# Optimization experiments

Hardware: AMD Instinct MI355X
Metric: run time of the kernel (lower is better)

The kernel has to match this reference:

```python
import jax, jax.numpy as jnp
import numpy as np

ALPHA = 0.15
CLIP = 5.0
EPS = 1e-6
LN_EPS = 1e-5

B, S, D, F = 4, 4096, 2048, 128


def setup_inputs() -> dict:
    key = jax.random.key(0)
    ks = jax.random.split(key, 8)
    sd = lambda fan_in: 1.0 / np.sqrt(fan_in)
    return {
        "x": jax.random.normal(ks[0], (B, S, D), dtype=jnp.float32),
        "Q_w": jax.random.normal(ks[1], (D, F), dtype=jnp.float32) * sd(D),
        "Q_b": jnp.zeros((F,), jnp.float32),
        "K_w": jax.random.normal(ks[2], (D, F), dtype=jnp.float32) * sd(D),
        "K_b": jnp.zeros((F,), jnp.float32),
        "lo_proj_w": jax.random.normal(ks[3], (D, D), dtype=jnp.float32) * sd(D),
        "lo_proj_b": jnp.zeros((D,), jnp.float32),
        "lo_p_w": jax.random.normal(ks[4], (D, F), dtype=jnp.float32) * sd(D),
        "lo_p_b": jnp.zeros((F,), jnp.float32),
        "proj_w": jax.random.normal(ks[5], (F, D), dtype=jnp.float32) * sd(F),
        "proj_b": jnp.zeros((D,), jnp.float32),
        "O_w": jax.random.normal(ks[6], (D // 2, D), dtype=jnp.float32) * sd(D // 2),
        "O_b": jnp.zeros((D,), jnp.float32),
        "ln_gamma": jnp.ones((D,), jnp.float32),
        "ln_beta": jnp.zeros((D,), jnp.float32),
    }


def _ema_over_time(score):
    # score: [B, S, F]; ema[0]=score[0]; ema[t]=a*score[t]+(1-a)*ema[t-1]
    seq = jnp.swapaxes(score, 0, 1)  # [S, B, F]

    def step(prev, x_t):
        new = ALPHA * x_t + (1.0 - ALPHA) * prev
        return new, new

    init = seq[0]
    _, rest = jax.lax.scan(step, init, seq[1:])
    ema_seq = jnp.concatenate([init[None], rest], axis=0)
    return jnp.swapaxes(ema_seq, 0, 1)


def reference(x, Q_w, Q_b, K_w, K_b, lo_proj_w, lo_proj_b, lo_p_w, lo_p_b,
              proj_w, proj_b, O_w, O_b, ln_gamma, ln_beta):
    x_f32 = x.astype(jnp.float32)
    residual = x_f32

    q = x_f32 @ Q_w + Q_b                    # [B,S,128]
    k = x_f32 @ K_w + K_b                    # [B,S,128]
    # Lo: Dense(d_model) -> gelu -> Dense(128)
    v_h = jax.nn.gelu(x_f32 @ lo_proj_w + lo_proj_b)
    V = v_h @ lo_p_w + lo_p_b                # [B,S,128]

    score = jax.nn.sigmoid(q) * jax.nn.sigmoid(k)
    score_ema = _ema_over_time(score)
    mean_last = jnp.mean(score_ema, axis=-1, keepdims=True)
    denom = jnp.maximum(mean_last, EPS)
    score_clipped = jnp.clip(score_ema / denom, -CLIP, CLIP)

    x_comb = score_clipped * V               # [B,S,128]
    out = x_comb @ proj_w + proj_b           # [B,S,D]  (D even -> no pad)
    a, b = jnp.split(out, 2, axis=-1)
    gated = jax.nn.silu(a) * b               # [B,S,D/2]
    out = gated @ O_w + O_b                  # [B,S,D]

    h = out + residual
    mu = jnp.mean(h, axis=-1, keepdims=True)
    var = jnp.var(h, axis=-1, keepdims=True)
    out = (h - mu) * jax.lax.rsqrt(var + LN_EPS) * ln_gamma + ln_beta
    return out.astype(x.dtype)
```

## Files before the change

### kernel.cpp

```cpp
#include <hip/hip_runtime.h>
#include <cstdint>

#define ALPHA_C 0.15f
#define ONE_MINUS_ALPHA 0.85f
#define CLIP_C 5.0f
#define EPS_C 1e-6f
#define LN_EPS_C 1e-5f

#define Bb 4
#define Ss 4096
#define Dd 2048
#define Mtot (Bb * Ss)

typedef __attribute__((ext_vector_type(8))) short bf16x8;
typedef __attribute__((ext_vector_type(4))) float f32x4;

__device__ __forceinline__ short f2bf(float f) {
  union { float f; uint32_t u; } v; v.f = f;
  uint32_t r = v.u + 0x7fffu + ((v.u >> 16) & 1u);
  return (short)(r >> 16);
}
__device__ __forceinline__ float sigf(float x) { return 1.0f / (1.0f + __expf(-x)); }
__device__ __forceinline__ float geluf(float x) {
  const float c = 0.7978845608028654f;
  float x3 = x * x * x;
  return 0.5f * x * (1.0f + tanhf(c * (x + 0.044715f * x3)));
}

__device__ __forceinline__ void load_lds16(const short* g, short* l) {
  __builtin_amdgcn_global_load_lds((__attribute__((address_space(1))) void*)g,
                                   (__attribute__((address_space(3))) void*)l, 16, 0, 0);
}

#define BM 128
#define BN 128
#define BK 32

template <int MODE>
__global__ __launch_bounds__(256, 4) void gemm_tn(
    const short* __restrict__ A, const short* __restrict__ Bt, void* __restrict__ out0,
    void* __restrict__ out1, const float* __restrict__ bias, int K, int lda, int ldb,
    int ldc, int nbx, long pstride) {
  __shared__ __align__(16) short As[BM * BK];
  __shared__ __align__(16) short Bs[BN * BK];

  const int tid = threadIdx.x;
  const int wave = tid >> 6;
  const int lane = tid & 63;
  const int quad = lane >> 4;
  const int l16 = lane & 15;

  const int bid = blockIdx.x;
  const int panel = bid / (8 * nbx);
  const int rem = bid - panel * (8 * nbx);
  const int by = panel * 8 + (rem & 7);
  const int bx = rem >> 3;
  const int m0 = by * BM;
  const int n0 = bx * BN;
  const int wm = (wave & 1) * 64;
  const int wn = (wave >> 1) * 64;

  if (MODE == 5) {
    A += (long)blockIdx.y * K;
    Bt += (long)blockIdx.y * K;
  }

  const int srow = wave * 32 + (lane >> 2);
  const int skoff = ((lane & 3) ^ ((lane >> 3) & 3)) * 8;
  const short* agp = A + (long)(m0 + srow) * lda + skoff;
  const short* bgp = Bt + (long)(n0 + srow) * ldb + skoff;
  const short* agp2 = agp + (long)16 * lda;
  const short* bgp2 = bgp + (long)16 * ldb;
  short* al = As + (wave * 32) * BK;
  short* al2 = al + 16 * BK;
  short* bl = Bs + (wave * 32) * BK;
  short* bl2 = bl + 16 * BK;

  const int rsw = (l16 >> 1) & 3;

  f32x4 acc[4][4] = {};

  for (int k0 = 0; k0 < K; k0 += BK) {
    __syncthreads();
    load_lds16(agp + k0, al);
    load_lds16(agp2 + k0, al2);
    load_lds16(bgp + k0, bl);
    load_lds16(bgp2 + k0, bl2);
    __syncthreads();

    bf16x8 af[4], bfr[4];
#pragma unroll
    for (int i = 0; i < 4; ++i)
      af[i] = *(const bf16x8*)&As[(wm + i * 16 + l16) * BK + (quad ^ rsw) * 8];
#pragma unroll
    for (int j = 0; j < 4; ++j)
      bfr[j] = *(const bf16x8*)&Bs[(wn + j * 16 + l16) * BK + (quad ^ rsw) * 8];
#pragma unroll
    for (int i = 0; i < 4; ++i)
#pragma unroll
      for (int j = 0; j < 4; ++j)
        acc[i][j] = __builtin_amdgcn_mfma_f32_16x16x32_bf16(af[i], bfr[j], acc[i][j], 0, 0, 0);
  }

#pragma unroll
  for (int i = 0; i < 4; ++i) {
#pragma unroll
    for (int r = 0; r < 4; ++r) {
      const int row = m0 + wm + i * 16 + quad * 4 + r;
#pragma unroll
      for (int j = 0; j < 4; ++j) {
        const int col = n0 + wn + j * 16 + l16;
        float v = acc[i][j][r];
        if (MODE != 5) v += bias[col];
        if (MODE == 0) {
          ((float*)out0)[(long)row * ldc + col] = v;
        } else if (MODE == 5) {
          float* o = (float*)out0 + (long)blockIdx.y * pstride;
          o[(long)row * ldc + col] = v;
        } else if (MODE == 3) {
          if (n0 < 256) {
            float sh = __shfl_xor(v, 1);
            if (!(lane & 1))
              ((float*)out0)[(long)row * 128 + (col >> 1)] = sigf(v) * sigf(sh);
          } else {
            ((short*)out1)[(long)row * 2048 + (col - 256)] = f2bf(geluf(v));
          }
        } else if (MODE == 4) {
          float sh = __shfl_xor(v, 1);
          if (!(lane & 1))
            ((short*)out0)[(long)row * 1024 + (col >> 1)] = f2bf(v * sigf(v) * sh);
        }
      }
    }
  }
}

__global__ __launch_bounds__(256) void cast_x_kernel(const float* __restrict__ in,
                                                     short* __restrict__ out, long n4) {
  long i = (long)blockIdx.x * blockDim.x + threadIdx.x;
  const long stride = (long)gridDim.x * blockDim.x;
  for (; i < n4; i += stride) {
    float4 v = ((const float4*)in)[i];
    short4 o;
    o.x = f2bf(v.x); o.y = f2bf(v.y); o.z = f2bf(v.z); o.w = f2bf(v.w);
    ((short4*)out)[i] = o;
  }
}

template <int MAP>
__global__ __launch_bounds__(256) void tcast_kernel(const float* __restrict__ in,
                                                    short* __restrict__ out, int R, int C) {
  __shared__ float t[32][33];
  const int c0 = blockIdx.x * 32, r0 = blockIdx.y * 32;
  const int tx = threadIdx.x, ty = threadIdx.y;
#pragma unroll
  for (int i = 0; i < 32; i += 8)
    t[ty + i][tx] = in[(long)(r0 + ty + i) * C + (c0 + tx)];
  __syncthreads();
#pragma unroll
  for (int i = 0; i < 32; i += 8) {
    const int c = c0 + ty + i;
    const int orow = (MAP == 0) ? c
                   : (MAP == 1) ? 2 * c
                   : (MAP == 2) ? 2 * c + 1
                                : (c < 1024 ? 2 * c : 2 * (c - 1024) + 1);
    out[(long)orow * R + (r0 + tx)] = f2bf(t[tx][ty + i]);
  }
}

__global__ void pack_bias_kernel(const float* __restrict__ qb, const float* __restrict__ kb,
                                 const float* __restrict__ lob, float* __restrict__ o) {
  int i = blockIdx.x * 256 + threadIdx.x;
  if (i < 256) o[i] = (i & 1) ? kb[i >> 1] : qb[i >> 1];
  else if (i < 2304) o[i] = lob[i - 256];
}
__global__ void pack_pbias_kernel(const float* __restrict__ pjb, float* __restrict__ o) {
  int i = blockIdx.x * 256 + threadIdx.x;
  o[i] = (i & 1) ? pjb[1024 + (i >> 1)] : pjb[i >> 1];
}

#define SEG 64
#define WARM 96
__global__ __launch_bounds__(128) void ema_kernel(const float* __restrict__ score,
                                                  float* __restrict__ ema) {
  const int f = threadIdx.x;
  const int b = blockIdx.y;
  const int seg = blockIdx.x;
  const int t0 = seg * SEG;
  const int tstart = (t0 >= WARM) ? (t0 - WARM) : 0;
  const int tend = t0 + SEG;
  const float* __restrict__ base = score + (long)b * Ss * 128;
  float* __restrict__ eb = ema + (long)b * Ss * 128;

  float e = base[(long)tstart * 128 + f];
  if (seg == 0) eb[f] = e;

  int t = tstart + 1;
  const int CH = 8;
  const int nch = (tend - t) / CH;
  float cur[CH];
#pragma unroll
  for (int i = 0; i < CH; ++i) cur[i] = ALPHA_C * base[(long)(t + i) * 128 + f];
  for (int c = 0; c < nch; ++c) {
    float nxt[CH] = {};
    if (c + 1 < nch) {
#pragma unroll
      for (int i = 0; i < CH; ++i) nxt[i] = ALPHA_C * base[(long)(t + CH + i) * 128 + f];
    }
#pragma unroll
    for (int i = 0; i < CH; ++i) {
      e = fmaf(ONE_MINUS_ALPHA, e, cur[i]);
      const int tt = t + i;
      if (tt >= t0) eb[(long)tt * 128 + f] = e;
    }
#pragma unroll
    for (int i = 0; i < CH; ++i) cur[i] = nxt[i];
    t += CH;
  }
  for (; t < tend; ++t) {
    e = fmaf(ONE_MINUS_ALPHA, e, ALPHA_C * base[(long)t * 128 + f]);
    if (t >= t0) eb[(long)t * 128 + f] = e;
  }
}

__global__ __launch_bounds__(256) void comb_kernel(const float* __restrict__ ema,
                                                   const float* __restrict__ vpart,
                                                   const float* __restrict__ lob,
                                                   short* __restrict__ xcomb) {
  const int wv = threadIdx.x >> 6;
  const int lane = threadIdx.x & 63;
  const long row = (long)blockIdx.x * 4 + wv;
  const float* er = ema + row * 128;
  float e0 = er[lane], e1 = er[lane + 64];
  float s = e0 + e1;
#pragma unroll
  for (int m = 1; m < 64; m <<= 1) s += __shfl_xor(s, m, 64);
  const float denom = fmaxf(s * (1.0f / 128.0f), EPS_C);
  const float inv = 1.0f / denom;
  const float c0 = fminf(fmaxf(e0 * inv, -CLIP_C), CLIP_C);
  const float c1 = fminf(fmaxf(e1 * inv, -CLIP_C), CLIP_C);
  const long PS = (long)Mtot * 128;
  float va = lob[lane], vb = lob[lane + 64];
#pragma unroll
  for (int p = 0; p < 4; ++p) {
    va += vpart[p * PS + row * 128 + lane];
    vb += vpart[p * PS + row * 128 + lane + 64];
  }
  xcomb[row * 128 + lane] = f2bf(c0 * va);
  xcomb[row * 128 + 64 + lane] = f2bf(c1 * vb);
}

__global__ __launch_bounds__(256) void ln_kernel(float* __restrict__ io,
                                                 const float* __restrict__ x,
                                                 const float* __restrict__ gamma,
                                                 const float* __restrict__ beta) {
  const long row = blockIdx.x;
  const int tid = threadIdx.x;
  const int wv = tid >> 6, lane = tid & 63;
  float* rp = io + row * 2048;
  const float* xp = x + row * 2048;
  float4 v0 = ((const float4*)rp)[tid * 2];
  float4 v1 = ((const float4*)rp)[tid * 2 + 1];
  float4 x0 = ((const float4*)xp)[tid * 2];
  float4 x1 = ((const float4*)xp)[tid * 2 + 1];
  float h[8] = {v0.x + x0.x, v0.y + x0.y, v0.z + x0.z, v0.w + x0.w,
                v1.x + x1.x, v1.y + x1.y, v1.z + x1.z, v1.w + x1.w};
  float sum = 0.f, ss = 0.f;
#pragma unroll
  for (int i = 0; i < 8; ++i) { sum += h[i]; ss += h[i] * h[i]; }
#pragma unroll
  for (int m = 1; m < 64; m <<= 1) {
    sum += __shfl_xor(sum, m, 64);
    ss += __shfl_xor(ss, m, 64);
  }
  __shared__ float rs[4], rq[4];
  if (lane == 0) { rs[wv] = sum; rq[wv] = ss; }
  __syncthreads();
  sum = rs[0] + rs[1] + rs[2] + rs[3];
  ss = rq[0] + rq[1] + rq[2] + rq[3];
  const float mu = sum * (1.0f / 2048.0f);
  const float var = ss * (1.0f / 2048.0f) - mu * mu;
  const float rstd = rsqrtf(var + LN_EPS_C);
  const int c0 = tid * 8;
  float o[8];
#pragma unroll
  for (int i = 0; i < 8; ++i)
    o[i] = (h[i] - mu) * rstd * gamma[c0 + i] + beta[c0 + i];
  ((float4*)rp)[tid * 2]     = make_float4(o[0], o[1], o[2], o[3]);
  ((float4*)rp)[tid * 2 + 1] = make_float4(o[4], o[5], o[6], o[7]);
}

extern "C" void kernel_launch(void* const* d_in, const int* in_sizes, int n_in,
                              void* d_out, int out_size, void* d_ws, size_t ws_size,
                              hipStream_t stream) {
  const float* x         = (const float*)d_in[0];
  const float* Q_w       = (const float*)d_in[1];
  const float* Q_b       = (const float*)d_in[2];
  const float* K_w       = (const float*)d_in[3];
  const float* K_b       = (const float*)d_in[4];
  const float* lo_proj_w = (const float*)d_in[5];
  const float* lo_proj_b = (const float*)d_in[6];
  const float* lo_p_w    = (const float*)d_in[7];
  const float* lo_p_b    = (const float*)d_in[8];
  const float* proj_w    = (const float*)d_in[9];
  const float* proj_b    = (const float*)d_in[10];
  const float* O_w       = (const float*)d_in[11];
  const float* O_b       = (const float*)d_in[12];
  const float* ln_g      = (const float*)d_in[13];
  const float* ln_b      = (const float*)d_in[14];

  char* ws = (char*)d_ws;
  size_t off = 0;
  auto alloc = [&](size_t bytes) {
    char* p = ws + off;
    off += (bytes + 255) & ~(size_t)255;
    return p;
  };
  short* x16   = (short*)alloc((size_t)Mtot * Dd * 2);
  short* h16   = (short*)alloc((size_t)Mtot * Dd * 2);
  float* score = (float*)alloc((size_t)Mtot * 128 * 4);
  float* emab  = (float*)alloc((size_t)Mtot * 128 * 4);
  short* xcomb = (short*)alloc((size_t)Mtot * 128 * 2);
  short* gated = (short*)alloc((size_t)Mtot * 1024 * 2);
  short* wbig  = (short*)alloc((size_t)2304 * 2048 * 2);
  short* lpt   = (short*)alloc((size_t)128 * 2048 * 2);
  short* prjt  = (short*)alloc((size_t)2048 * 128 * 2);
  short* ot    = (short*)alloc((size_t)2048 * 1024 * 2);
  float* biasb = (float*)alloc(2304 * 4);
  float* pbias = (float*)alloc(2048 * 4);
  float* vpart = (float*)x16;
  float* outf  = (float*)d_out;

  cast_x_kernel<<<8192, 256, 0, stream>>>(x, x16, (long)Mtot * Dd / 4);
  tcast_kernel<1><<<dim3(4, 64), dim3(32, 8), 0, stream>>>(Q_w, wbig, 2048, 128);
  tcast_kernel<2><<<dim3(4, 64), dim3(32, 8), 0, stream>>>(K_w, wbig, 2048, 128);
  tcast_kernel<0><<<dim3(64, 64), dim3(32, 8), 0, stream>>>(lo_proj_w, wbig + 256 * 2048, 2048, 2048);
  tcast_kernel<0><<<dim3(4, 64), dim3(32, 8), 0, stream>>>(lo_p_w, lpt, 2048, 128);
  tcast_kernel<3><<<dim3(64, 4), dim3(32, 8), 0, stream>>>(proj_w, prjt, 128, 2048);
  tcast_kernel<0><<<dim3(64, 32), dim3(32, 8), 0, stream>>>(O_w, ot, 1024, 2048);
  pack_bias_kernel<<<9, 256, 0, stream>>>(Q_b, K_b, lo_proj_b, biasb);
  pack_pbias_kernel<<<8, 256, 0, stream>>>(proj_b, pbias);

  gemm_tn<3><<<18 * 128, 256, 0, stream>>>(x16, wbig, score, h16, biasb,
                                           2048, 2048, 2048, 0, 18, 0);
  ema_kernel<<<dim3(Ss / SEG, 4), 128, 0, stream>>>(score, emab);
  gemm_tn<5><<<dim3(128, 4), 256, 0, stream>>>(h16, lpt, vpart, nullptr, nullptr,
                                               512, 2048, 2048, 128, 1, (long)Mtot * 128);
  comb_kernel<<<Mtot / 4, 256, 0, stream>>>(emab, vpart, lo_p_b, xcomb);
  gemm_tn<4><<<16 * 128, 256, 0, stream>>>(xcomb, prjt, gated, nullptr, pbias,
                                           128, 128, 128, 1024, 16, 0);
  gemm_tn<0><<<16 * 128, 256, 0, stream>>>(gated, ot, outf, nullptr, O_b,
                                           1024, 1024, 1024, 2048, 16, 0);
  ln_kernel<<<Mtot, 256, 0, stream>>>(outf, x, ln_g, ln_b);
}
```

Measured before the change: 719.1 us.

## Add 256x256-tile double-buffered MFMA GEMM for the two large projections

Adds a new gemm256 kernel that uses 256x256 output tiles with 512 threads, BK=64, XOR-swizzled LDS, double-buffered global-to-LDS loads, and MFMA phases interleaved with barriers and setprio. The big fused Q/K/lo_proj GEMM and the O projection GEMM are switched to this kernel with an L2-friendly block swizzle. The aim is higher arithmetic intensity and better latency hiding than the 128x128 gemm_tn. In exchange it needs 128KB of LDS and many accumulator registers per block, which limits occupancy.

```diff
diff --git a/kernel.cpp b/kernel.cpp
--- a/kernel.cpp
+++ b/kernel.cpp
@@ -30,6 +30,127 @@
 __device__ __forceinline__ void load_lds16(const short* g, short* l) {
   __builtin_amdgcn_global_load_lds((__attribute__((address_space(1))) void*)g,
                                    (__attribute__((address_space(3))) void*)l, 16, 0, 0);
+}
+
+#define RD_A(KK)                                                                     \
+  _Pragma("unroll") for (int m = 0; m < 8; ++m)                                      \
+      a[m] = *(const bf16x8*)&Ab[(wr128 + m * 16 + l16) * 64 +                       \
+                                 ((((KK) * 4 + quad) ^ key) * 8)];
+#define RD_B(KK)                                                                     \
+  _Pragma("unroll") for (int n = 0; n < 4; ++n)                                      \
+      bfr[KK][n] = *(const bf16x8*)&Bb2[(wc64 + n * 16 + l16) * 64 +                 \
+                                        ((((KK) * 4 + quad) ^ key) * 8)];
+#define MFMA_PH(KK, NB)                                                              \
+  __builtin_amdgcn_s_setprio(1);                                                     \
+  _Pragma("unroll") for (int m = 0; m < 8; ++m) {                                    \
+    acc[m][NB] = __builtin_amdgcn_mfma_f32_16x16x32_bf16(a[m], bfr[KK][NB],          \
+                                                         acc[m][NB], 0, 0, 0);       \
+    acc[m][NB + 1] = __builtin_amdgcn_mfma_f32_16x16x32_bf16(a[m], bfr[KK][NB + 1],  \
+                                                             acc[m][NB + 1], 0, 0, 0);\
+  }                                                                                  \
+  __builtin_amdgcn_s_setprio(0);
+#define BARF()                                                                       \
+  {                                                                                  \
+    asm volatile("" ::: "memory");                                                   \
+    __builtin_amdgcn_s_barrier();                                                    \
+    asm volatile("" ::: "memory");                                                   \
+  }
+#define STAGE(tt)                                                                    \
+  {                                                                                  \
+    short* ls = smem + ((tt) & 1) * 32768;                                           \
+    const long co = (long)(tt) * 64;                                                 \
+    _Pragma("unroll") for (int i = 0; i < 4; ++i)                                    \
+        load_lds16(baseA + (long)i * 64 * lda + co, ls + (i * 64 + w * 8) * 64);     \
+    _Pragma("unroll") for (int i = 0; i < 4; ++i)                                    \
+        load_lds16(baseB + (long)i * 64 * ldb + co,                                  \
+                   ls + 16384 + (i * 64 + w * 8) * 64);                              \
+  }
+
+template <int MODE>
+__global__ __launch_bounds__(512, 2) void gemm256(
+    const short* __restrict__ A, const short* __restrict__ Bt, void* __restrict__ out0,
+    void* __restrict__ out1, const float* __restrict__ bias, int K, int lda, int ldb,
+    int ldc, int nbx) {
+  __shared__ short smem[65536];
+
+  const int tid = threadIdx.x;
+  const int w = tid >> 6;
+  const int lane = tid & 63;
+  const int quad = lane >> 4;
+  const int l16 = lane & 15;
+  const int key = l16 & 7;
+  const int wr = w >> 2;
+  const int wc = w & 3;
+  const int wr128 = wr * 128;
+  const int wc64 = wc * 64;
+
+  const int nwg = gridDim.x;
+  const int swz = (blockIdx.x & 7) * (nwg >> 3) + (blockIdx.x >> 3);
+  const int by = swz / nbx;
+  const int bx = swz - by * nbx;
+  const int m0 = by * 256;
+  const int n0 = bx * 256;
+
+  const int srow = w * 8 + (lane >> 3);
+  const int schunk = (lane & 7) ^ (lane >> 3);
+  const short* baseA = A + (long)(m0 + srow) * lda + schunk * 8;
+  const short* baseB = Bt + (long)(n0 + srow) * ldb + schunk * 8;
+
+  const int NT = K >> 6;
+
+  f32x4 acc[8][4] = {};
+  bf16x8 a[8], bfr[2][4];
+
+  STAGE(0);
+
+  for (int t = 0; t < NT; ++t) {
+    const short* Ab = smem + (t & 1) * 32768;
+    const short* Bb2 = Ab + 16384;
+    if (t + 1 < NT) {
+      STAGE(t + 1);
+      asm volatile("s_waitcnt vmcnt(8)" ::: "memory");
+    } else {
+      asm volatile("s_waitcnt vmcnt(0)" ::: "memory");
+    }
+    __builtin_amdgcn_s_barrier();
+    asm volatile("" ::: "memory");
+    RD_A(0);
+    RD_B(0);
+    MFMA_PH(0, 0);
+    BARF();
+    RD_B(1);
+    MFMA_PH(0, 2);
+    BARF();
+    RD_A(1);
+    MFMA_PH(1, 0);
+    BARF();
+    MFMA_PH(1, 2);
+    BARF();
+  }
+
+#pragma unroll
+  for (int m = 0; m < 8; ++m) {
+#pragma unroll
+    for (int r = 0; r < 4; ++r) {
+      const int row = m0 + wr128 + m * 16 + quad * 4 + r;
+#pragma unroll
+      for (int n = 0; n < 4; ++n) {
+        const int col = n0 + wc64 + n * 16 + l16;
+        float v = acc[m][n][r] + bias[col];
+        if (MODE == 0) {
+          ((float*)out0)[(long)row * ldc + col] = v;
+        } else {
+          if (n0 == 0) {
+            float sh = __shfl_xor(v, 1);
+            if (!(lane & 1))
+              ((float*)out0)[(long)row * 128 + (col >> 1)] = sigf(v) * sigf(sh);
+          } else {
+            ((short*)out1)[(long)row * 2048 + (col - 256)] = f2bf(geluf(v));
+          }
+        }
+      }
+    }
+  }
 }
 
 #define BM 128
@@ -341,15 +462,15 @@
   pack_bias_kernel<<<9, 256, 0, stream>>>(Q_b, K_b, lo_proj_b, biasb);
   pack_pbias_kernel<<<8, 256, 0, stream>>>(proj_b, pbias);
 
-  gemm_tn<3><<<18 * 128, 256, 0, stream>>>(x16, wbig, score, h16, biasb,
-                                           2048, 2048, 2048, 0, 18, 0);
+  gemm256<3><<<576, 512, 0, stream>>>(x16, wbig, score, h16, biasb,
+                                      2048, 2048, 2048, 0, 9);
   ema_kernel<<<dim3(Ss / SEG, 4), 128, 0, stream>>>(score, emab);
   gemm_tn<5><<<dim3(128, 4), 256, 0, stream>>>(h16, lpt, vpart, nullptr, nullptr,
                                                512, 2048, 2048, 128, 1, (long)Mtot * 128);
   comb_kernel<<<Mtot / 4, 256, 0, stream>>>(emab, vpart, lo_p_b, xcomb);
   gemm_tn<4><<<16 * 128, 256, 0, stream>>>(xcomb, prjt, gated, nullptr, pbias,
                                            128, 128, 128, 1024, 16, 0);
-  gemm_tn<0><<<16 * 128, 256, 0, stream>>>(gated, ot, outf, nullptr, O_b,
-                                           1024, 1024, 1024, 2048, 16, 0);
+  gemm256<0><<<512, 512, 0, stream>>>(gated, ot, outf, nullptr, O_b,
+                                      1024, 1024, 1024, 2048, 8);
   ln_kernel<<<Mtot, 256, 0, stream>>>(outf, x, ln_g, ln_b);
 }
```

Measured after the change: 745.8 us. +3.7%, slower.
